# Optimization experiments

Hardware: AMD Instinct MI355X
Metric: run time of the kernel (lower is better)

Reference implementation:

```python
import jax, jax.numpy as jnp
from jax import lax
import numpy as np

B, T, F = 256, 256, 40
H, A, HORIZON = 256, 64, 60
D_SP = 192


def setup_inputs() -> dict:
    key = jax.random.key(0)
    ks = jax.random.split(key, 16)
    s = 0.05  # weight scale to keep activations stable
    return {
        'x': jax.random.normal(ks[0], (B, T, F), jnp.float32),
        'W_sp': jax.random.normal(ks[1], (F, D_SP), jnp.float32) * s,
        'b_sp': jnp.zeros((D_SP,), jnp.float32),
        'Wx_ef': jax.random.normal(ks[2], (D_SP, 4 * H), jnp.float32) * s,
        'Wh_ef': jax.random.normal(ks[3], (H, 4 * H), jnp.float32) * s,
        'b_ef': jnp.zeros((4 * H,), jnp.float32),
        'Wx_eb': jax.random.normal(ks[4], (D_SP, 4 * H), jnp.float32) * s,
        'Wh_eb': jax.random.normal(ks[5], (H, 4 * H), jnp.float32) * s,
        'b_eb': jnp.zeros((4 * H,), jnp.float32),
        'We': jax.random.normal(ks[6], (2 * H, A), jnp.float32) * s,
        'Wd': jax.random.normal(ks[7], (H, A), jnp.float32) * s,
        'v': jax.random.normal(ks[8], (A,), jnp.float32) * s,
        'Wx_d': jax.random.normal(ks[9], (1 + 2 * H, 4 * H), jnp.float32) * s,
        'Wh_d': jax.random.normal(ks[10], (H, 4 * H), jnp.float32) * s,
        'b_d': jnp.zeros((4 * H,), jnp.float32),
        'W_ih': jax.random.normal(ks[11], (2 * H, H), jnp.float32) * s,
        'b_ih': jnp.zeros((H,), jnp.float32),
        'W_ic': jax.random.normal(ks[12], (2 * H, H), jnp.float32) * s,
        'b_ic': jnp.zeros((H,), jnp.float32),
        'Wo': jax.random.normal(ks[13], (H, 1), jnp.float32) * s,
        'bo': jnp.zeros((1,), jnp.float32),
    }


def _lstm_cell(x_t, h, c, Wx, Wh, b):
    g = x_t @ Wx + h @ Wh + b
    i, f, gg, o = jnp.split(g, 4, axis=-1)  # torch gate order i,f,g,o
    c = jax.nn.sigmoid(f) * c + jax.nn.sigmoid(i) * jnp.tanh(gg)
    h = jax.nn.sigmoid(o) * jnp.tanh(c)
    return h, c


def _lstm_scan(xs_tbd, Wx, Wh, b):
    # xs_tbd: [T, B, D] -> hs [T, B, H]
    h0 = jnp.zeros((xs_tbd.shape[1], Wh.shape[0]), xs_tbd.dtype)
    c0 = jnp.zeros_like(h0)
    def step(carry, x_t):
        h, c = carry
        h, c = _lstm_cell(x_t, h, c, Wx, Wh, b)
        return (h, c), h
    _, hs = lax.scan(step, (h0, c0), xs_tbd)
    return hs


def reference(x, W_sp, b_sp, Wx_ef, Wh_ef, b_ef, Wx_eb, Wh_eb, b_eb,
              We, Wd, v, Wx_d, Wh_d, b_d, W_ih, b_ih, W_ic, b_ic, Wo, bo):
    # spatial encoder (stand-in for DeepLOBEncoder): [B,T,F] -> [B,T,192]
    h_spatial = x @ W_sp + b_sp
    xs = jnp.swapaxes(h_spatial, 0, 1)          # [T, B, 192]
    hs_f = _lstm_scan(xs, Wx_ef, Wh_ef, b_ef)    # [T, B, H]
    hs_b = _lstm_scan(xs[::-1], Wx_eb, Wh_eb, b_eb)[::-1]
    enc_out = jnp.swapaxes(jnp.concatenate([hs_f, hs_b], axis=-1), 0, 1)  # [B,T,2H]

    enc_mean = enc_out.mean(axis=1)
    dec_h = jnp.tanh(enc_mean @ W_ih + b_ih)     # [B, H]
    dec_c = jnp.tanh(enc_mean @ W_ic + b_ic)

    enc_proj = enc_out @ We                      # [B, T, A] precomputed (same math)
    prev_y = ((x[:, -1, 0] + x[:, -1, 2]) / 2.0)[:, None]  # ask_idx=0, bid_idx=2

    def dec_step(carry, _):
        h, c, py = carry
        e = jnp.tanh(enc_proj + (h @ Wd)[:, None, :])        # [B,T,A]
        scores = e @ v                                        # [B,T]
        w = jax.nn.softmax(scores, axis=1)
        context = jnp.einsum('bt,bth->bh', w, enc_out)        # [B,2H]
        dec_in = jnp.concatenate([py, context], axis=1)       # [B,1+2H]
        h, c = _lstm_cell(dec_in, h, c, Wx_d, Wh_d, b_d)
        y = h @ Wo + bo                                       # [B,1]
        return (h, c, lax.stop_gradient(y)), y[:, 0]

    _, ys = lax.scan(dec_step, (dec_h, dec_c, prev_y), None, length=HORIZON)
    return jnp.swapaxes(ys, 0, 1)  # [B, horizon]
```

## Files before the change

kernel.cpp:

```cpp
#include <hip/hip_runtime.h>
#include <cmath>

#define B_ 256
#define T_ 256
#define F_ 40
#define H_ 256
#define A_ 64
#define HOR_ 60
#define DSP_ 192
#define ENC_NBLK 128
#define GRP_SZ 16
#define WSTR 456
#define FPAD 32
#define ADLD 1024
#define CT 56

typedef unsigned short u16;
typedef unsigned int u32;
typedef __attribute__((ext_vector_type(8))) short bf16x8;
typedef __attribute__((ext_vector_type(4))) float f32x4;
typedef __attribute__((ext_vector_type(8))) u32 u32x8;
typedef __attribute__((ext_vector_type(4))) u32 u32x4;

__device__ __forceinline__ float sigm(float x){ return 1.f/(1.f+expf(-x)); }

__device__ __forceinline__ u16 f2bf(float x){
  u32 u = __float_as_uint(x);
  u32 r = (u + 0x7FFFu + ((u>>16)&1u)) >> 16;
  return (u16)r;
}
__device__ __forceinline__ float bf2f(u16 h){ return __uint_as_float(((u32)h)<<16); }
__device__ __forceinline__ u32 packsplit(float x){
  u16 hi = f2bf(x);
  u16 lo = f2bf(x - bf2f(hi));
  return (u32)hi | ((u32)lo<<16);
}
__device__ __forceinline__ float unpack2f(u32 v){
  return __uint_as_float(v<<16) + __uint_as_float(v & 0xFFFF0000u);
}

__device__ __forceinline__ float wred_sum(float v){
  #pragma unroll
  for (int o=32;o>0;o>>=1) v += __shfl_xor(v,o);
  return v;
}
__device__ __forceinline__ float wred_max(float v){
  #pragma unroll
  for (int o=32;o>0;o>>=1) v = fmaxf(v,__shfl_xor(v,o));
  return v;
}

__device__ __forceinline__ void cnt_signal(int* c){
  __hip_atomic_fetch_add(c, 1, __ATOMIC_RELEASE, __HIP_MEMORY_SCOPE_AGENT);
}
__device__ __forceinline__ void cnt_wait(const int* c, int n, int tid){
  if (tid == 0){
    while (__hip_atomic_load(c, __ATOMIC_ACQUIRE, __HIP_MEMORY_SCOPE_AGENT) < n)
      __builtin_amdgcn_s_sleep(1);
  }
  __syncthreads();
}

__global__ void conv_w(const float* __restrict__ Wx, const float* __restrict__ Wh,
                       u16* __restrict__ hi, u16* __restrict__ lo,
                       int KX, int Ktot, int N){
  int idx = blockIdx.x*256 + threadIdx.x;
  if (idx >= N*Ktot) return;
  int n = idx / Ktot, k = idx - n*Ktot;
  float w = (k < KX) ? Wx[(size_t)k*N + n] : Wh[(size_t)(k-KX)*N + n];
  u16 h = f2bf(w);
  hi[idx] = h;
  lo[idx] = f2bf(w - bf2f(h));
}

__global__ __launch_bounds__(192) void spatial_proj(
    const float* __restrict__ x, const float* __restrict__ W, const float* __restrict__ bsp,
    u32* __restrict__ hsp32){
  __shared__ float Ws[40][192];
  __shared__ float xr[40];
  int t = blockIdx.x, tid = threadIdx.x;
  for (int i = tid; i < 40*192; i += 192){ int k = i/192, c = i-k*192; Ws[k][c] = W[i]; }
  float bb = bsp[tid];
  __syncthreads();
  for (int b=0; b<B_; b++){
    if (tid < 40) xr[tid] = x[((size_t)b*T_ + t)*F_ + tid];
    __syncthreads();
    float acc = bb;
    #pragma unroll
    for (int k=0;k<40;k++) acc += xr[k]*Ws[k][tid];
    hsp32[((size_t)t*B_ + b)*DSP_ + tid] = packsplit(acc);
    __syncthreads();
  }
}

__global__ __launch_bounds__(256) void enc_scan(
    const u32* __restrict__ hsp32,
    const u16* __restrict__ W_hi, const u16* __restrict__ W_lo,
    const float* __restrict__ b_ef, const float* __restrict__ b_eb,
    u32* __restrict__ hbuf, u32* __restrict__ eo32, int* __restrict__ bar)
{
  extern __shared__ u16 smem[];
  u16* Whi = smem;
  u16* Wlo = smem + 4*16*WSTR;
  const int bid = blockIdx.x;
  const int grp = bid & 7;
  const int nt  = bid >> 3;
  const int dir = grp >> 2;
  const int m0  = (grp & 3) * 64;
  const int u0  = nt * 16;
  const int tid = threadIdx.x;
  const int wave = tid >> 6, lane = tid & 63;
  const int lrow = lane & 15, kblk = lane >> 4;
  const int koff = kblk * 8;
  {
    const size_t wbase = ((size_t)dir*1024 + u0) * 448;
    for (int idx = tid; idx < 4*16*448; idx += 256){
      int g = idx / (16*448);
      int r = idx - g*(16*448);
      int j = r / 448;
      int k = r - j*448;
      size_t go = wbase + ((size_t)g*256 + j)*448 + k;
      Whi[(g*16 + j)*WSTR + k] = W_hi[go];
      Wlo[(g*16 + j)*WSTR + k] = W_lo[go];
    }
  }
  const float* bias = dir ? b_eb : b_ef;
  float bg4[4];
  #pragma unroll
  for (int g=0; g<4; g++) bg4[g] = bias[g*H_ + u0 + lrow];
  __syncthreads();

  const int mrow = m0 + wave*16;
  const int arow = mrow + lrow;
  u32* hP0 = hbuf + (size_t)dir*(B_*H_);
  u32* hP1 = hbuf + (size_t)(2+dir)*(B_*H_);
  int* gbar = bar + grp*T_;
  float c_reg[4] = {0.f,0.f,0.f,0.f};

  for (int s=0; s<T_; s++){
    const int t = dir ? (T_-1-s) : s;
    f32x4 acc[4] = {};
    const u32* abase = hsp32 + ((size_t)t*B_ + arow)*DSP_;
    #pragma unroll
    for (int ks=0; ks<6; ks++){
      int kb = ks*32 + koff;
      u32x8 la = *(const u32x8*)(abase + kb);
      bf16x8 ah, al;
      #pragma unroll
      for (int j=0;j<8;j++){ ah[j]=(short)(la[j]&0xFFFFu); al[j]=(short)(la[j]>>16); }
      #pragma unroll
      for (int g=0; g<4; g++){
        bf16x8 bh = *(const bf16x8*)(Whi + (g*16+lrow)*WSTR + kb);
        bf16x8 bl = *(const bf16x8*)(Wlo + (g*16+lrow)*WSTR + kb);
        acc[g] = __builtin_amdgcn_mfma_f32_16x16x32_bf16(ah, bh, acc[g], 0,0,0);
        acc[g] = __builtin_amdgcn_mfma_f32_16x16x32_bf16(ah, bl, acc[g], 0,0,0);
        acc[g] = __builtin_amdgcn_mfma_f32_16x16x32_bf16(al, bh, acc[g], 0,0,0);
      }
    }
    if (s > 0){
      if (tid == 0){
        while (__hip_atomic_load(&gbar[s-1], __ATOMIC_ACQUIRE, __HIP_MEMORY_SCOPE_AGENT) < GRP_SZ)
          __builtin_amdgcn_s_sleep(1);
      }
      __syncthreads();
    }
    const u32* hin = (s & 1) ? hP1 : hP0;
    u32* hout      = (s & 1) ? hP0 : hP1;
    const u32* hbase = hin + (size_t)arow*H_;
    #pragma unroll
    for (int ks=0; ks<8; ks++){
      int kb = ks*32 + koff;
      u32x8 la = *(const u32x8*)(hbase + kb);
      bf16x8 ah, al;
      #pragma unroll
      for (int j=0;j<8;j++){ ah[j]=(short)(la[j]&0xFFFFu); al[j]=(short)(la[j]>>16); }
      #pragma unroll
      for (int g=0; g<4; g++){
        bf16x8 bh = *(const bf16x8*)(Whi + (g*16+lrow)*WSTR + 192 + kb);
        bf16x8 bl = *(const bf16x8*)(Wlo + (g*16+lrow)*WSTR + 192 + kb);
        acc[g] = __builtin_amdgcn_mfma_f32_16x16x32_bf16(ah, bh, acc[g], 0,0,0);
        acc[g] = __builtin_amdgcn_mfma_f32_16x16x32_bf16(ah, bl, acc[g], 0,0,0);
        acc[g] = __builtin_amdgcn_mfma_f32_16x16x32_bf16(al, bh, acc[g], 0,0,0);
      }
    }
    #pragma unroll
    for (int r=0; r<4; r++){
      int brow = mrow + kblk*4 + r;
      float gi = acc[0][r] + bg4[0];
      float gf = acc[1][r] + bg4[1];
      float gg = acc[2][r] + bg4[2];
      float go = acc[3][r] + bg4[3];
      float cn = sigm(gf)*c_reg[r] + sigm(gi)*tanhf(gg);
      float hn = sigm(go)*tanhf(cn);
      c_reg[r] = cn;
      u32 hp = packsplit(hn);
      hout[(size_t)brow*H_ + u0 + lrow] = hp;
      eo32[((size_t)brow*T_ + t)*512 + dir*H_ + u0 + lrow] = hp;
    }
    if (s == T_-1) break;
    __syncthreads();
    if (tid == 0)
      __hip_atomic_fetch_add(&gbar[s], 1, __ATOMIC_RELEASE, __HIP_MEMORY_SCOPE_AGENT);
  }
}

__global__ __launch_bounds__(512) void dec_scan(
    const u32* __restrict__ eo32,
    const u16* __restrict__ Wet_hi, const u16* __restrict__ Wet_lo,
    const float* __restrict__ W_ih, const float* __restrict__ b_ih,
    const float* __restrict__ W_ic, const float* __restrict__ b_ic,
    const float* __restrict__ x, float* __restrict__ ep,
    const float* __restrict__ Wd, const float* __restrict__ v,
    const float* __restrict__ Wo, const float* __restrict__ bo,
    const u16* __restrict__ W_hi, const u16* __restrict__ W_lo,
    const float* __restrict__ b_d, const float* __restrict__ Wx_d,
    float* __restrict__ hdp, float* __restrict__ cd,
    u32* __restrict__ Ad32, float* __restrict__ py,
    float* __restrict__ out, int* __restrict__ cntA, int* __restrict__ cntB)
{
  __shared__ float sh_h[256], sh_hwd[64], sh_v[64], sh_sc[256], sh_w[256];
  __shared__ float red8[8][64];
  __shared__ float sh_red[4], sh_red2[4];
  __shared__ float redc[8][512];
  __shared__ float gl[8][16][16];
  __shared__ float em_s[512];
  __shared__ u32 eoL[CT*512];
  const int b = blockIdx.x, tid = threadIdx.x;
  const int wave = tid >> 6, lane = tid & 63;
  const int bx = b & 15, by = b >> 4;
  const int cr = tid >> 4, cu = tid & 15;
  float c_reg = 0.f;
  float bg0=0,bg1=0,bg2=0,bg3=0, w00=0,w01=0,w02=0,w03=0;
  if (tid < 256){
    int uu = bx*16 + cu;
    bg0 = b_d[uu];       bg1 = b_d[256+uu];
    bg2 = b_d[512+uu];   bg3 = b_d[768+uu];
    w00 = Wx_d[uu];      w01 = Wx_d[256+uu];
    w02 = Wx_d[512+uu];  w03 = Wx_d[768+uu];
  }
  {
    const u32* src = eo32 + (size_t)b*T_*512;
    for (int i = tid; i < CT*512/4; i += 512)
      ((u32x4*)eoL)[i] = *(const u32x4*)(src + (size_t)i*4);
  }
  {
    const int lrow = lane & 15, kblk = lane >> 4, koff = kblk*8;
    #pragma unroll
    for (int mi=0; mi<2; mi++){
      int mt = wave*2 + mi;
      f32x4 acc[4] = {};
      for (int ks=0; ks<16; ks++){
        int kb = ks*32 + koff;
        u32x8 ld = *(const u32x8*)(eo32 + ((size_t)b*T_ + mt*16 + lrow)*512 + kb);
        bf16x8 ah, al;
        #pragma unroll
        for (int j=0;j<8;j++){ ah[j]=(short)(ld[j]&0xFFFFu); al[j]=(short)(ld[j]>>16); }
        #pragma unroll
        for (int nf=0; nf<4; nf++){
          bf16x8 bh = *(const bf16x8*)(Wet_hi + (size_t)(nf*16+lrow)*512 + kb);
          bf16x8 bl = *(const bf16x8*)(Wet_lo + (size_t)(nf*16+lrow)*512 + kb);
          acc[nf] = __builtin_amdgcn_mfma_f32_16x16x32_bf16(ah, bh, acc[nf], 0,0,0);
          acc[nf] = __builtin_amdgcn_mfma_f32_16x16x32_bf16(ah, bl, acc[nf], 0,0,0);
          acc[nf] = __builtin_amdgcn_mfma_f32_16x16x32_bf16(al, bh, acc[nf], 0,0,0);
        }
      }
      #pragma unroll
      for (int nf=0; nf<4; nf++)
        #pragma unroll
        for (int r=0; r<4; r++)
          ep[((size_t)b*T_ + mt*16 + kblk*4 + r)*64 + nf*16 + lrow] = acc[nf][r];
    }
  }
  {
    float cacc[8] = {};
    const u32* eo = eo32 + (size_t)b*T_*512 + lane*8;
    #pragma unroll 8
    for (int tt=0; tt<32; tt++){
      int t = wave*32 + tt;
      u32x4 e0 = *(const u32x4*)(eo + (size_t)t*512);
      u32x4 e1 = *(const u32x4*)(eo + (size_t)t*512 + 4);
      #pragma unroll
      for (int j=0;j<4;j++){ cacc[j] += unpack2f(e0[j]); cacc[4+j] += unpack2f(e1[j]); }
    }
    #pragma unroll
    for (int j=0;j<8;j++) redc[wave][lane*8+j] = cacc[j];
    __syncthreads();
    if (tid < 256){
      float s0=0.f, s1=0.f;
      #pragma unroll
      for (int q=0;q<8;q++){ s0 += redc[q][tid]; s1 += redc[q][256+tid]; }
      em_s[tid] = s0*(1.f/T_); em_s[256+tid] = s1*(1.f/T_);
    }
    __syncthreads();
  }
  if (tid < 256){
    float ah = b_ih[tid], ac = b_ic[tid];
    for (int k=0;k<512;k++){
      float e = em_s[k];
      ah += e*W_ih[(size_t)k*256 + tid];
      ac += e*W_ic[(size_t)k*256 + tid];
    }
    float h0 = tanhf(ah), c0 = tanhf(ac);
    sh_h[tid] = h0;
    hdp[(size_t)b*H_ + tid] = h0;
    Ad32[(size_t)b*ADLD + 512 + tid] = packsplit(h0);
    cd[(size_t)b*H_ + tid] = c0;
  }
  if (tid == 0){
    size_t xb = ((size_t)b*T_ + 255)*F_;
    py[b] = (x[xb] + x[xb+2])*0.5f;
  }
  if (tid >= 448) sh_v[tid-448] = v[tid-448];
  __syncthreads();
  for (int s=0; s<=HOR_; s++){
    if (s > 0){
      cnt_wait(cntB + (size_t)((s-1)*16 + by)*FPAD, 16, tid);
      if (tid < 256) sh_h[tid] = hdp[(size_t)(s&1)*B_*H_ + (size_t)b*H_ + tid];
      __syncthreads();
      if (tid < 256){
        float p = sh_h[tid] * Wo[tid];
        p = wred_sum(p);
        if ((tid & 63) == 0) sh_red[tid>>6] = p;
      }
      __syncthreads();
      if (tid == 0){
        float y = sh_red[0]+sh_red[1]+sh_red[2]+sh_red[3] + bo[0];
        out[b*HOR_ + (s-1)] = y;
        py[b] = y;
      }
    }
    if (s == HOR_) break;
    {
      float ssum = 0.f;
      for (int j=wave*32; j<wave*32+32; j++) ssum += sh_h[j]*Wd[(size_t)j*A_ + lane];
      red8[wave][lane] = ssum;
      __syncthreads();
      if (tid < 64){
        float a = 0.f;
        #pragma unroll
        for (int q=0;q<8;q++) a += red8[q][tid];
        sh_hwd[tid] = a;
      }
    }
    __syncthreads();
    {
      int t = tid >> 1, aa = tid & 1;
      const float4* ep4 = (const float4*)(ep + ((size_t)(b*T_+t))*A_ + aa*32);
      float partial = 0.f;
      #pragma unroll
      for (int q=0;q<8;q++){
        float4 e4 = ep4[q];
        int a0 = aa*32 + q*4;
        partial += tanhf(e4.x + sh_hwd[a0+0]) * sh_v[a0+0];
        partial += tanhf(e4.y + sh_hwd[a0+1]) * sh_v[a0+1];
        partial += tanhf(e4.z + sh_hwd[a0+2]) * sh_v[a0+2];
        partial += tanhf(e4.w + sh_hwd[a0+3]) * sh_v[a0+3];
      }
      partial += __shfl_xor(partial, 1);
      if (aa == 0) sh_sc[t] = partial;
    }
    __syncthreads();
    if (tid < 256){
      float sc = sh_sc[tid];
      float m = wred_max(sc);
      if ((tid&63)==0) sh_red[tid>>6] = m;
      __syncthreads();
      m = fmaxf(fmaxf(sh_red[0],sh_red[1]), fmaxf(sh_red[2],sh_red[3]));
      float e = expf(sc - m);
      float su = wred_sum(e);
      if ((tid&63)==0) sh_red2[tid>>6] = su;
      __syncthreads();
      su = (sh_red2[0]+sh_red2[1])+(sh_red2[2]+sh_red2[3]);
      sh_w[tid] = e / su;
    } else { __syncthreads(); __syncthreads(); }
    __syncthreads();
    {
      float cacc[8] = {};
      const int t0 = wave*32, t1 = t0 + 32;
      const int tL = (t1 < CT) ? t1 : CT;
      for (int t=t0; t<tL; ++t){
        float wgt = sh_w[t];
        const u32* p = eoL + t*512 + lane*8;
        u32x4 e0 = *(const u32x4*)p;
        u32x4 e1 = *(const u32x4*)(p + 4);
        #pragma unroll
        for (int j=0;j<4;j++){
          cacc[j]   += wgt * unpack2f(e0[j]);
          cacc[4+j] += wgt * unpack2f(e1[j]);
        }
      }
      const u32* eo = eo32 + (size_t)b*T_*512 + lane*8;
      const int tG = (t0 > CT) ? t0 : CT;
      #pragma unroll 4
      for (int t=tG; t<t1; ++t){
        float wgt = sh_w[t];
        u32x4 e0 = *(const u32x4*)(eo + (size_t)t*512);
        u32x4 e1 = *(const u32x4*)(eo + (size_t)t*512 + 4);
        #pragma unroll
        for (int j=0;j<4;j++){
          cacc[j]   += wgt * unpack2f(e0[j]);
          cacc[4+j] += wgt * unpack2f(e1[j]);
        }
      }
      #pragma unroll
      for (int j=0;j<8;j++) redc[wave][lane*8+j] = cacc[j];
    }
    __syncthreads();
    if (tid < 256){
      float c0 = 0.f, c1 = 0.f;
      #pragma unroll
      for (int q=0;q<8;q++){ c0 += redc[q][tid]; c1 += redc[q][256+tid]; }
      Ad32[(size_t)b*ADLD + tid]       = packsplit(c0);
      Ad32[(size_t)b*ADLD + 256 + tid] = packsplit(c1);
    }
    __syncthreads();
    if (tid == 0)
      cnt_signal(cntA + (size_t)(s*16 + by)*FPAD);
    cnt_wait(cntA + (size_t)(s*16 + by)*FPAD, 16, tid);
    if (s == 0 && tid < 256)
      c_reg = cd[(size_t)(by*16 + cr)*H_ + bx*16 + cu];
    const int par = s & 1;
    {
      const int g = wave & 3, kh = wave >> 2;
      const int r16 = lane & 15, kb4 = lane >> 4;
      f32x4 acc = {0.f,0.f,0.f,0.f};
      const u32* ar = Ad32 + (size_t)(by*16 + r16)*ADLD;
      const u16* WH = W_hi + (size_t)(g*256 + bx*16 + r16)*768;
      const u16* WL = W_lo + (size_t)(g*256 + bx*16 + r16)*768;
      for (int ks=kh*12; ks<kh*12+12; ks++){
        int kb = ks*32 + kb4*8;
        int kp = (kb < 512) ? kb : (kb + (par<<8));
        u32x8 ld = *(const u32x8*)(ar + kp);
        bf16x8 ah, al;
        #pragma unroll
        for (int j=0;j<8;j++){ ah[j]=(short)(ld[j]&0xFFFFu); al[j]=(short)(ld[j]>>16); }
        bf16x8 bh = *(const bf16x8*)(WH + kb);
        bf16x8 bl = *(const bf16x8*)(WL + kb);
        acc = __builtin_amdgcn_mfma_f32_16x16x32_bf16(ah, bh, acc, 0,0,0);
        acc = __builtin_amdgcn_mfma_f32_16x16x32_bf16(ah, bl, acc, 0,0,0);
        acc = __builtin_amdgcn_mfma_f32_16x16x32_bf16(al, bh, acc, 0,0,0);
      }
      #pragma unroll
      for (int vv=0; vv<4; vv++) gl[wave][kb4*4+vv][r16] = acc[vv];
    }
    __syncthreads();
    if (tid < 256){
      float pyr = py[by*16 + cr];
      float gi = gl[0][cr][cu] + gl[4][cr][cu] + bg0 + pyr*w00;
      float gf = gl[1][cr][cu] + gl[5][cr][cu] + bg1 + pyr*w01;
      float gg = gl[2][cr][cu] + gl[6][cr][cu] + bg2 + pyr*w02;
      float go = gl[3][cr][cu] + gl[7][cr][cu] + bg3 + pyr*w03;
      float cn = sigm(gf)*c_reg + sigm(gi)*tanhf(gg);
      float hn = sigm(go)*tanhf(cn);
      c_reg = cn;
      size_t ridx = (size_t)(by*16+cr)*H_ + bx*16+cu;
      hdp[(size_t)((s+1)&1)*B_*H_ + ridx] = hn;
      Ad32[(size_t)(by*16+cr)*ADLD + 512 + (((s+1)&1)<<8) + bx*16+cu] = packsplit(hn);
    }
    __syncthreads();
    if (tid == 0)
      cnt_signal(cntB + (size_t)(s*16 + by)*FPAD);
  }
}

extern "C" void kernel_launch(void* const* d_in, const int* in_sizes, int n_in,
                              void* d_out, int out_size, void* d_ws, size_t ws_size,
                              hipStream_t stream)
{
  const float* x    = (const float*)d_in[0];
  const float* W_sp = (const float*)d_in[1];
  const float* b_sp = (const float*)d_in[2];
  const float* Wx_ef= (const float*)d_in[3];
  const float* Wh_ef= (const float*)d_in[4];
  const float* b_ef = (const float*)d_in[5];
  const float* Wx_eb= (const float*)d_in[6];
  const float* Wh_eb= (const float*)d_in[7];
  const float* b_eb = (const float*)d_in[8];
  const float* We   = (const float*)d_in[9];
  const float* Wd   = (const float*)d_in[10];
  const float* v    = (const float*)d_in[11];
  const float* Wx_d = (const float*)d_in[12];
  const float* Wh_d = (const float*)d_in[13];
  const float* b_d  = (const float*)d_in[14];
  const float* W_ih = (const float*)d_in[15];
  const float* b_ih = (const float*)d_in[16];
  const float* W_ic = (const float*)d_in[17];
  const float* b_ic = (const float*)d_in[18];
  const float* Wo   = (const float*)d_in[19];
  const float* bo   = (const float*)d_in[20];
  float* out = (float*)d_out;

  char* base = (char*)d_ws;
  auto alloc = [&](size_t bytes)->char*{
    char* p = base; base += (bytes + 255) & ~(size_t)255; return p;
  };
  u16* Wenc_hi = (u16*)alloc((size_t)2*1024*448*2);
  u16* Wenc_lo = (u16*)alloc((size_t)2*1024*448*2);
  u16* Wdec_hi = (u16*)alloc((size_t)1024*768*2);
  u16* Wdec_lo = (u16*)alloc((size_t)1024*768*2);
  u16* Wet_hi  = (u16*)alloc((size_t)64*512*2);
  u16* Wet_lo  = (u16*)alloc((size_t)64*512*2);
  u32* hsp32   = (u32*)alloc((size_t)T_*B_*DSP_*4);
  u32* hbuf    = (u32*)alloc((size_t)2*2*B_*H_*4);
  u32* eo32    = (u32*)alloc((size_t)B_*T_*512*4);
  float* ep    = (float*)alloc((size_t)B_*T_*64*4);
  float* cd    = (float*)alloc((size_t)B_*H_*4);
  float* hdp   = (float*)alloc((size_t)2*B_*H_*4);
  u32* Ad32    = (u32*)alloc((size_t)B_*ADLD*4);
  float* pyb   = (float*)alloc((size_t)B_*4);
  int* bar     = (int*)alloc((size_t)8*T_*4);
  int* cntA    = (int*)alloc((size_t)HOR_*16*FPAD*4);
  int* cntB    = (int*)alloc((size_t)HOR_*16*FPAD*4);
  if ((size_t)(base - (char*)d_ws) > ws_size) return;

  conv_w<<<dim3(1792),256,0,stream>>>(Wx_ef, Wh_ef, Wenc_hi, Wenc_lo, DSP_, 448, 1024);
  conv_w<<<dim3(1792),256,0,stream>>>(Wx_eb, Wh_eb, Wenc_hi+458752, Wenc_lo+458752, DSP_, 448, 1024);
  conv_w<<<dim3(3072),256,0,stream>>>(Wx_d+1024, Wh_d, Wdec_hi, Wdec_lo, 512, 768, 1024);
  conv_w<<<dim3(128),256,0,stream>>>(We, We, Wet_hi, Wet_lo, 512, 512, 64);

  spatial_proj<<<dim3(256),192,0,stream>>>(x, W_sp, b_sp, hsp32);

  hipMemsetAsync(hbuf, 0, (size_t)2*B_*H_*4, stream);
  hipMemsetAsync(bar, 0, (size_t)8*T_*4, stream);
  hipMemsetAsync(cntA, 0, (size_t)HOR_*16*FPAD*4, stream);
  hipMemsetAsync(cntB, 0, (size_t)HOR_*16*FPAD*4, stream);

  enc_scan<<<dim3(ENC_NBLK), dim3(256), 2*4*16*WSTR*2, stream>>>(
      hsp32, Wenc_hi, Wenc_lo, b_ef, b_eb, hbuf, eo32, bar);

  dec_scan<<<dim3(256),512,0,stream>>>(
      eo32, Wet_hi, Wet_lo, W_ih, b_ih, W_ic, b_ic, x, ep,
      Wd, v, Wo, bo, Wdec_hi, Wdec_lo, b_d, Wx_d,
      hdp, cd, Ad32, pyb, out, cntA, cntB);
}
```

Baseline: 5.555 ms.

## Cache more encoder outputs in LDS and registers for decoder attention context

Raises the LDS-resident slice of encoder outputs in the decoder from 56 to 64 timesteps. Waves 2-7 also keep 16 timesteps each in registers (eoR) across all horizon steps, which cuts global memory reads in the per-step context reduction. To fit this, the redc and gl shared buffers merge into one smaller buffer, and the cross-wave reduction is split into two halves with extra barriers. launch_bounds(512,2) is added, which limits registers per thread and may cause spills given the 128 registers of cached data.

```diff
diff --git a/kernel.cpp b/kernel.cpp
--- a/kernel.cpp
+++ b/kernel.cpp
@@ -13,7 +13,8 @@
 #define WSTR 456
 #define FPAD 32
 #define ADLD 1024
-#define CT 56
+#define CT 64
+#define RR 16
 
 typedef unsigned short u16;
 typedef unsigned int u32;
@@ -204,7 +205,7 @@
   }
 }
 
-__global__ __launch_bounds__(512) void dec_scan(
+__global__ __launch_bounds__(512,2) void dec_scan(
     const u32* __restrict__ eo32,
     const u16* __restrict__ Wet_hi, const u16* __restrict__ Wet_lo,
     const float* __restrict__ W_ih, const float* __restrict__ b_ih,
@@ -221,8 +222,7 @@
   __shared__ float sh_h[256], sh_hwd[64], sh_v[64], sh_sc[256], sh_w[256];
   __shared__ float red8[8][64];
   __shared__ float sh_red[4], sh_red2[4];
-  __shared__ float redc[8][512];
-  __shared__ float gl[8][16][16];
+  __shared__ float shun[8][256];
   __shared__ float em_s[512];
   __shared__ u32 eoL[CT*512];
   const int b = blockIdx.x, tid = threadIdx.x;
@@ -282,14 +282,28 @@
       #pragma unroll
       for (int j=0;j<4;j++){ cacc[j] += unpack2f(e0[j]); cacc[4+j] += unpack2f(e1[j]); }
     }
-    #pragma unroll
-    for (int j=0;j<8;j++) redc[wave][lane*8+j] = cacc[j];
+    if (lane < 32){
+      #pragma unroll
+      for (int j=0;j<8;j++) shun[wave][lane*8+j] = cacc[j];
+    }
     __syncthreads();
     if (tid < 256){
-      float s0=0.f, s1=0.f;
-      #pragma unroll
-      for (int q=0;q<8;q++){ s0 += redc[q][tid]; s1 += redc[q][256+tid]; }
-      em_s[tid] = s0*(1.f/T_); em_s[256+tid] = s1*(1.f/T_);
+      float s0=0.f;
+      #pragma unroll
+      for (int q=0;q<8;q++) s0 += shun[q][tid];
+      em_s[tid] = s0*(1.f/T_);
+    }
+    __syncthreads();
+    if (lane >= 32){
+      #pragma unroll
+      for (int j=0;j<8;j++) shun[wave][(lane-32)*8+j] = cacc[j];
+    }
+    __syncthreads();
+    if (tid < 256){
+      float s1=0.f;
+      #pragma unroll
+      for (int q=0;q<8;q++) s1 += shun[q][tid];
+      em_s[256+tid] = s1*(1.f/T_);
     }
     __syncthreads();
   }
@@ -311,6 +325,12 @@
     py[b] = (x[xb] + x[xb+2])*0.5f;
   }
   if (tid >= 448) sh_v[tid-448] = v[tid-448];
+  u32x8 eoR[RR];
+  if (wave >= 2){
+    const u32* srcR = eo32 + ((size_t)b*T_ + wave*32)*512 + lane*8;
+    #pragma unroll
+    for (int r=0;r<RR;r++) eoR[r] = *(const u32x8*)(srcR + (size_t)r*512);
+  }
   __syncthreads();
   for (int s=0; s<=HOR_; s++){
     if (s > 0){
@@ -376,42 +396,62 @@
     __syncthreads();
     {
       float cacc[8] = {};
-      const int t0 = wave*32, t1 = t0 + 32;
-      const int tL = (t1 < CT) ? t1 : CT;
-      for (int t=t0; t<tL; ++t){
-        float wgt = sh_w[t];
-        const u32* p = eoL + t*512 + lane*8;
-        u32x4 e0 = *(const u32x4*)p;
-        u32x4 e1 = *(const u32x4*)(p + 4);
-        #pragma unroll
-        for (int j=0;j<4;j++){
-          cacc[j]   += wgt * unpack2f(e0[j]);
-          cacc[4+j] += wgt * unpack2f(e1[j]);
+      if (wave < 2){
+        for (int tt=0; tt<32; ++tt){
+          int t = wave*32 + tt;
+          float wgt = sh_w[t];
+          const u32* p = eoL + t*512 + lane*8;
+          u32x4 e0 = *(const u32x4*)p;
+          u32x4 e1 = *(const u32x4*)(p + 4);
+          #pragma unroll
+          for (int j=0;j<4;j++){
+            cacc[j]   += wgt * unpack2f(e0[j]);
+            cacc[4+j] += wgt * unpack2f(e1[j]);
+          }
         }
-      }
-      const u32* eo = eo32 + (size_t)b*T_*512 + lane*8;
-      const int tG = (t0 > CT) ? t0 : CT;
-      #pragma unroll 4
-      for (int t=tG; t<t1; ++t){
-        float wgt = sh_w[t];
-        u32x4 e0 = *(const u32x4*)(eo + (size_t)t*512);
-        u32x4 e1 = *(const u32x4*)(eo + (size_t)t*512 + 4);
-        #pragma unroll
-        for (int j=0;j<4;j++){
-          cacc[j]   += wgt * unpack2f(e0[j]);
-          cacc[4+j] += wgt * unpack2f(e1[j]);
+      } else {
+        #pragma unroll
+        for (int r=0;r<RR;r++){
+          float wgt = sh_w[wave*32 + r];
+          #pragma unroll
+          for (int j=0;j<8;j++) cacc[j] += wgt * unpack2f(eoR[r][j]);
         }
-      }
-      #pragma unroll
-      for (int j=0;j<8;j++) redc[wave][lane*8+j] = cacc[j];
-    }
-    __syncthreads();
-    if (tid < 256){
-      float c0 = 0.f, c1 = 0.f;
-      #pragma unroll
-      for (int q=0;q<8;q++){ c0 += redc[q][tid]; c1 += redc[q][256+tid]; }
-      Ad32[(size_t)b*ADLD + tid]       = packsplit(c0);
-      Ad32[(size_t)b*ADLD + 256 + tid] = packsplit(c1);
+        const u32* eo = eo32 + (size_t)b*T_*512 + lane*8;
+        #pragma unroll 4
+        for (int t=wave*32+RR; t<wave*32+32; ++t){
+          float wgt = sh_w[t];
+          u32x4 e0 = *(const u32x4*)(eo + (size_t)t*512);
+          u32x4 e1 = *(const u32x4*)(eo + (size_t)t*512 + 4);
+          #pragma unroll
+          for (int j=0;j<4;j++){
+            cacc[j]   += wgt * unpack2f(e0[j]);
+            cacc[4+j] += wgt * unpack2f(e1[j]);
+          }
+        }
+      }
+      if (lane < 32){
+        #pragma unroll
+        for (int j=0;j<8;j++) shun[wave][lane*8+j] = cacc[j];
+      }
+      __syncthreads();
+      if (tid < 256){
+        float c0 = 0.f;
+        #pragma unroll
+        for (int q=0;q<8;q++) c0 += shun[q][tid];
+        Ad32[(size_t)b*ADLD + tid] = packsplit(c0);
+      }
+      __syncthreads();
+      if (lane >= 32){
+        #pragma unroll
+        for (int j=0;j<8;j++) shun[wave][(lane-32)*8+j] = cacc[j];
+      }
+      __syncthreads();
+      if (tid < 256){
+        float c1 = 0.f;
+        #pragma unroll
+        for (int q=0;q<8;q++) c1 += shun[q][tid];
+        Ad32[(size_t)b*ADLD + 256 + tid] = packsplit(c1);
+      }
     }
     __syncthreads();
     if (tid == 0)
@@ -441,15 +481,15 @@
         acc = __builtin_amdgcn_mfma_f32_16x16x32_bf16(al, bh, acc, 0,0,0);
       }
       #pragma unroll
-      for (int vv=0; vv<4; vv++) gl[wave][kb4*4+vv][r16] = acc[vv];
+      for (int vv=0; vv<4; vv++) shun[wave][(kb4*4+vv)*16 + r16] = acc[vv];
     }
     __syncthreads();
     if (tid < 256){
       float pyr = py[by*16 + cr];
-      float gi = gl[0][cr][cu] + gl[4][cr][cu] + bg0 + pyr*w00;
-      float gf = gl[1][cr][cu] + gl[5][cr][cu] + bg1 + pyr*w01;
-      float gg = gl[2][cr][cu] + gl[6][cr][cu] + bg2 + pyr*w02;
-      float go = gl[3][cr][cu] + gl[7][cr][cu] + bg3 + pyr*w03;
+      float gi = shun[0][cr*16+cu] + shun[4][cr*16+cu] + bg0 + pyr*w00;
+      float gf = shun[1][cr*16+cu] + shun[5][cr*16+cu] + bg1 + pyr*w01;
+      float gg = shun[2][cr*16+cu] + shun[6][cr*16+cu] + bg2 + pyr*w02;
+      float go = shun[3][cr*16+cu] + shun[7][cr*16+cu] + bg3 + pyr*w03;
       float cn = sigm(gf)*c_reg + sigm(gi)*tanhf(gg);
       float hn = sigm(go)*tanhf(cn);
       c_reg = cn;
```

Result: slower. 5.781 ms (+4.1%).
